# Performance work log

Hardware: AMD Instinct MI355X
Metric: run time of the kernel (lower is better)

## Reference

```python
import jax, jax.numpy as jnp
import numpy as np

B, T, C, H = 4, 2048, 1024, 16
HD = C // H
INIT_SCALE = 0.25

def setup_inputs() -> dict:
    key = jax.random.key(0)
    k1, k2, k3 = jax.random.split(key, 3)
    x = jax.random.normal(k1, (B, T, C), dtype=jnp.float32)
    W_attn = jax.random.normal(k2, (3 * C, C), dtype=jnp.float32) * INIT_SCALE  # torch Linear weight [out,in]
    b_attn = jnp.zeros((3 * C,), dtype=jnp.float32)
    W_proj = jax.random.normal(k3, (C, C), dtype=jnp.float32) * INIT_SCALE
    b_proj = jnp.zeros((C,), dtype=jnp.float32)
    return {"x": x, "W_attn": W_attn, "b_attn": b_attn, "W_proj": W_proj, "b_proj": b_proj}

def reference(x, W_attn, b_attn, W_proj, b_proj):
    # fused QKV projection: [B,T,3C]
    qkv = x @ W_attn.T + b_attn
    q, k, v = jnp.split(qkv, 3, axis=-1)  # each [B,T,C]
    # [B,H,T,HD]
    q = q.reshape(B, T, H, HD).transpose(0, 2, 1, 3)
    k = k.reshape(B, T, H, HD).transpose(0, 2, 1, 3)
    v = v.reshape(B, T, H, HD).transpose(0, 2, 1, 3)
    scale = 1.0 / jnp.sqrt(jnp.asarray(HD, dtype=q.dtype))
    attn = jnp.einsum('bhqd,bhkd->bhqk', q, k) * scale  # [B,H,T,T]
    attn = jax.nn.softmax(attn, axis=-1)
    out = jnp.einsum('bhqk,bhkd->bhqd', attn, v)  # [B,H,T,HD]
    out = out.transpose(0, 2, 1, 3).reshape(B, T, C)
    return out @ W_proj.T + b_proj
```

## Files before the change

### kernel.cpp

```cpp
#include <hip/hip_runtime.h>
#include <hip/hip_bf16.h>

#define BB 4
#define TT 2048
#define CC 1024
#define HH 16
#define HD 64

typedef _Float16 half8 __attribute__((ext_vector_type(8)));
typedef _Float16 half4 __attribute__((ext_vector_type(4)));
typedef _Float16 half2_t __attribute__((ext_vector_type(2)));
typedef __fp16 fp16x2 __attribute__((ext_vector_type(2)));
typedef float floatx4 __attribute__((ext_vector_type(4)));
typedef float floatx16 __attribute__((ext_vector_type(16)));
typedef int intx2 __attribute__((ext_vector_type(2)));
typedef int intx4 __attribute__((ext_vector_type(4)));

__device__ __forceinline__ void async_cp16(const void* g, void* l) {
    __builtin_amdgcn_global_load_lds(
        (const __attribute__((address_space(1))) unsigned int*)g,
        (__attribute__((address_space(3))) unsigned int*)l,
        16, 0, 0);
}

__device__ __forceinline__ float exp2_raw(float x) {
    return __builtin_amdgcn_exp2f(x);
}

__device__ __forceinline__ int pkh(float a, float b) {
    fp16x2 v = __builtin_amdgcn_cvt_pkrtz(a, b);
    return __builtin_bit_cast(int, v);
}

__device__ __forceinline__ float maxv16(floatx16 s) {
    float a0 = fmaxf(fmaxf(s[0], s[1]), s[2]);
    float a1 = fmaxf(fmaxf(s[3], s[4]), s[5]);
    float a2 = fmaxf(fmaxf(s[6], s[7]), s[8]);
    float a3 = fmaxf(fmaxf(s[9], s[10]), s[11]);
    float a4 = fmaxf(fmaxf(s[12], s[13]), s[14]);
    float b0 = fmaxf(fmaxf(a0, a1), a2);
    float b1 = fmaxf(fmaxf(a3, a4), s[15]);
    return fmaxf(b0, b1);
}

__device__ __forceinline__ half8 assembleF(int a, int b, int c, int d) {
    intx2 s1 = __builtin_amdgcn_permlane32_swap(a, c, false, false);
    intx2 s2 = __builtin_amdgcn_permlane32_swap(b, d, false, false);
    intx4 w = {s1[0], s2[0], s1[1], s2[1]};
    return __builtin_bit_cast(half8, w);
}

#define NX  (BB * TT * CC)
#define NWA (3 * CC * CC)
#define NWP (CC * CC)
__global__ void cvt_all(const float* __restrict__ x, const float* __restrict__ wa,
                        const float* __restrict__ wp,
                        _Float16* __restrict__ xh, _Float16* __restrict__ wah,
                        _Float16* __restrict__ wph) {
    int i = (blockIdx.x * blockDim.x + threadIdx.x) * 8;
    const float* src;
    _Float16* dst;
    int j;
    if (i < NX)            { src = x;  dst = xh;  j = i; }
    else if (i < NX + NWA) { src = wa; dst = wah; j = i - NX; }
    else                   { src = wp; dst = wph; j = i - NX - NWA; }
    float4 v0 = *(const float4*)(src + j);
    float4 v1 = *(const float4*)(src + j + 4);
    half8 h;
    h[0] = (_Float16)v0.x; h[1] = (_Float16)v0.y; h[2] = (_Float16)v0.z; h[3] = (_Float16)v0.w;
    h[4] = (_Float16)v1.x; h[5] = (_Float16)v1.y; h[6] = (_Float16)v1.z; h[7] = (_Float16)v1.w;
    *(half8*)(dst + j) = h;
}

template <int EPI>
__global__ __launch_bounds__(256) void hgemm_nt(
    const _Float16* __restrict__ A, const _Float16* __restrict__ Bw,
    const float* __restrict__ bias,
    _Float16* __restrict__ q_out, _Float16* __restrict__ k_out, _Float16* __restrict__ v_out,
    float* __restrict__ c_out,
    int M, int N, int K)
{
    __shared__ __attribute__((aligned(16))) _Float16 As[2 * 128 * 32];
    __shared__ __attribute__((aligned(16))) _Float16 Bs[2 * 128 * 32];

    const int tid  = threadIdx.x;
    const int lane = tid & 63;
    const int wave = tid >> 6;
    const int quad = lane >> 4;
    const int lc   = lane & 15;
    const int wr   = wave >> 1, wc = wave & 1;

    const int nwg = gridDim.x * gridDim.y;
    int flat = blockIdx.y * gridDim.x + blockIdx.x;
    flat = (flat & 7) * (nwg >> 3) + (flat >> 3);
    const size_t bm = (size_t)(flat / gridDim.x) * 128;
    const size_t bn = (size_t)(flat % gridDim.x) * 128;

    const int r0 = tid >> 2;
    const int ck = (tid & 3) * 8;

    const _Float16* Ap = A + (bm + r0) * (size_t)K + ck;
    const _Float16* Bp = Bw + (bn + r0) * (size_t)K + ck;
    _Float16* lA = As + tid * 8;
    _Float16* lB = Bs + tid * 8;
    const size_t rstep = (size_t)64 * K;

    floatx4 acc[4][4] = {};

    for (int kk = 0; kk < K; kk += 64) {
        __syncthreads();
        async_cp16(Ap + kk, lA);
        async_cp16(Ap + kk + rstep, lA + 2048);
        async_cp16(Ap + kk + 32, lA + 4096);
        async_cp16(Ap + kk + 32 + rstep, lA + 4096 + 2048);
        async_cp16(Bp + kk, lB);
        async_cp16(Bp + kk + rstep, lB + 2048);
        async_cp16(Bp + kk + 32, lB + 4096);
        async_cp16(Bp + kk + 32 + rstep, lB + 4096 + 2048);
        __syncthreads();

#pragma unroll
        for (int h = 0; h < 2; h++) {
            half8 af[4], bf[4];
#pragma unroll
            for (int mt = 0; mt < 4; mt++)
                af[mt] = *(const half8*)(As + h * 4096 + (wr * 64 + mt * 16 + lc) * 32 + quad * 8);
#pragma unroll
            for (int nt = 0; nt < 4; nt++)
                bf[nt] = *(const half8*)(Bs + h * 4096 + (wc * 64 + nt * 16 + lc) * 32 + quad * 8);
#pragma unroll
            for (int mt = 0; mt < 4; mt++)
#pragma unroll
                for (int nt = 0; nt < 4; nt++)
                    acc[mt][nt] = __builtin_amdgcn_mfma_f32_16x16x32_f16(af[mt], bf[nt], acc[mt][nt], 0, 0, 0);
        }
    }

#pragma unroll
    for (int mt = 0; mt < 4; mt++) {
        int mbase = (int)bm + wr * 64 + mt * 16 + quad * 4;
#pragma unroll
        for (int nt = 0; nt < 4; nt++) {
            int n = (int)bn + wc * 64 + nt * 16 + lc;
            float bv = bias[n];
#pragma unroll
            for (int r = 0; r < 4; r++) {
                float v = acc[mt][nt][r] + bv;
                int mm = mbase + r;
                if (EPI == 0) {
                    int seg = n >> 10;
                    int cm  = n & 1023;
                    int h = cm >> 6, d = cm & 63;
                    int bb = mm >> 11, t = mm & 2047;
                    size_t dst = (((size_t)(bb * HH + h)) * TT + t) * HD + d;
                    if (seg == 0)      q_out[dst] = (_Float16)(v * 0.18033688f);
                    else if (seg == 1) k_out[dst] = (_Float16)v;
                    else               v_out[dst] = (_Float16)v;
                } else {
                    c_out[(size_t)mm * N + n] = v;
                }
            }
        }
    }
}

__global__ __launch_bounds__(512) void attn_flash(
    const _Float16* __restrict__ Qp, const _Float16* __restrict__ Kp,
    const _Float16* __restrict__ Vp, _Float16* __restrict__ Op)
{
    __shared__ __attribute__((aligned(16))) _Float16 Ks[2][64 * 64];
    __shared__ __attribute__((aligned(16))) _Float16 Vt[2][64 * 64];

    const int bh   = blockIdx.x;
    const int qt   = blockIdx.y;
    const int tid  = threadIdx.x;
    const int lane = tid & 63;
    const int wave = tid >> 6;
    const int ql   = lane & 31;
    const int hi   = lane >> 5;

    const size_t hb = (size_t)bh * TT * HD;

    const int qrow = qt * 256 + wave * 32 + ql;
    half8 bq[4];
#pragma unroll
    for (int c = 0; c < 4; c++)
        bq[c] = *(const half8*)(Qp + hb + (size_t)qrow * HD + c * 16 + hi * 8);

    floatx16 o0 = (floatx16)0.0f, o1 = (floatx16)0.0f;
    float mrun = -1e30f, lrun = 0.f;

    const int sk = tid >> 3;
    const int sj = tid & 7;
    const int sg = sj ^ (sk & 7);
    const _Float16* Kg = Kp + hb + (size_t)sk * HD + sg * 8;

    const int vkp = tid >> 4;
    const int vd4 = (tid & 15) * 4;
    const _Float16* Vg0 = Vp + hb + (size_t)(2 * vkp) * HD + vd4;
    const _Float16* Vg1 = Vg0 + HD;

    half8 kv  = *(const half8*)Kg;
    half4 va0 = *(const half4*)Vg0;
    half4 vb0 = *(const half4*)Vg1;
    *(half8*)(Ks[0] + tid * 8) = kv;
#pragma unroll
    for (int j = 0; j < 4; j++) {
        int row = vd4 + j;
        int boff = (row * 128 + vkp * 4) ^ (((row >> 2) & 7) << 4);
        half2_t w; w[0] = va0[j]; w[1] = vb0[j];
        *(half2_t*)((char*)Vt[0] + boff) = w;
    }
    {
        const size_t koff = (size_t)64 * HD;
        kv  = *(const half8*)(Kg + koff);
        va0 = *(const half4*)(Vg0 + koff);
        vb0 = *(const half4*)(Vg1 + koff);
    }

    int cur = 0;
    for (int kt = 0; kt < TT; kt += 64) {
        __syncthreads();

        if (kt + 64 < TT) {
            *(half8*)(Ks[cur ^ 1] + tid * 8) = kv;
#pragma unroll
            for (int j = 0; j < 4; j++) {
                int row = vd4 + j;
                int boff = (row * 128 + vkp * 4) ^ (((row >> 2) & 7) << 4);
                half2_t w; w[0] = va0[j]; w[1] = vb0[j];
                *(half2_t*)((char*)Vt[cur ^ 1] + boff) = w;
            }
            if (kt + 128 < TT) {
                const size_t koff = (size_t)(kt + 128) * HD;
                kv  = *(const half8*)(Kg + koff);
                va0 = *(const half4*)(Vg0 + koff);
                vb0 = *(const half4*)(Vg1 + koff);
            }
        }

        const char* Kbuf = (const char*)Ks[cur];
        const char* Vbuf = (const char*)Vt[cur];

        floatx16 s0 = (floatx16)0.0f, s1 = (floatx16)0.0f;
        __builtin_amdgcn_s_setprio(1);
#pragma unroll
        for (int c = 0; c < 4; c++) {
            int offk = (ql * 128 + c * 32 + hi * 16) ^ ((ql & 7) << 4);
            half8 a0 = *(const half8*)(Kbuf + offk);
            half8 a1 = *(const half8*)(Kbuf + offk + 4096);
            s0 = __builtin_amdgcn_mfma_f32_32x32x16_f16(a0, bq[c], s0, 0, 0, 0);
            s1 = __builtin_amdgcn_mfma_f32_32x32x16_f16(a1, bq[c], s1, 0, 0, 0);
        }
        __builtin_amdgcn_s_setprio(0);

        float mx = fmaxf(maxv16(s0), maxv16(s1));
        mx = fmaxf(mx, __shfl_xor(mx, 32));
        const bool noresc = __all(mx <= mrun + 8.0f);
        const float mnew = noresc ? mrun : fmaxf(mrun, mx);
        float rs = 0.f;
        int d[16];
#pragma unroll
        for (int i = 0; i < 8; i++) {
            float e0 = exp2_raw(s0[2 * i] - mnew);
            float e1 = exp2_raw(s0[2 * i + 1] - mnew);
            rs += e0 + e1;
            d[i] = pkh(e0, e1);
        }
#pragma unroll
        for (int i = 0; i < 8; i++) {
            float e0 = exp2_raw(s1[2 * i] - mnew);
            float e1 = exp2_raw(s1[2 * i + 1] - mnew);
            rs += e0 + e1;
            d[8 + i] = pkh(e0, e1);
        }
        rs += __shfl_xor(rs, 32);
        if (!noresc) {
            float al = exp2_raw(mrun - mnew);
            mrun = mnew;
            lrun *= al;
            o0 *= al;
            o1 *= al;
        }
        lrun += rs;

        half8 F[4];
        F[0] = assembleF(d[0], d[1], d[2], d[3]);
        F[1] = assembleF(d[4], d[5], d[6], d[7]);
        F[2] = assembleF(d[8], d[9], d[10], d[11]);
        F[3] = assembleF(d[12], d[13], d[14], d[15]);

        __builtin_amdgcn_s_setprio(1);
#pragma unroll
        for (int kb = 0; kb < 4; kb++) {
            int offv = (ql * 128 + kb * 32 + hi * 16) ^ (((ql >> 2) & 7) << 4);
            half8 v0 = *(const half8*)(Vbuf + offv);
            half8 v1 = *(const half8*)(Vbuf + offv + 4096);
            o0 = __builtin_amdgcn_mfma_f32_32x32x16_f16(v0, F[kb], o0, 0, 0, 0);
            o1 = __builtin_amdgcn_mfma_f32_32x32x16_f16(v1, F[kb], o1, 0, 0, 0);
        }
        __builtin_amdgcn_s_setprio(0);

        cur ^= 1;
    }

    const float inv = __builtin_amdgcn_rcpf(lrun);
    const int b = bh >> 4, h = bh & 15;
    size_t base = ((size_t)(b * TT + qrow)) * CC + h * HD;
#pragma unroll
    for (int rr = 0; rr < 4; rr++) {
        half4 hv0, hv1;
#pragma unroll
        for (int t = 0; t < 4; t++) {
            hv0[t] = (_Float16)(o0[rr * 4 + t] * inv);
            hv1[t] = (_Float16)(o1[rr * 4 + t] * inv);
        }
        *(half4*)(Op + base + 8 * rr + 4 * hi) = hv0;
        *(half4*)(Op + base + 32 + 8 * rr + 4 * hi) = hv1;
    }
}

extern "C" void kernel_launch(void* const* d_in, const int* in_sizes, int n_in,
                              void* d_out, int out_size, void* d_ws, size_t ws_size,
                              hipStream_t stream) {
    const float* x      = (const float*)d_in[0];
    const float* W_attn = (const float*)d_in[1];
    const float* b_attn = (const float*)d_in[2];
    const float* W_proj = (const float*)d_in[3];
    const float* b_proj = (const float*)d_in[4];
    float* out = (float*)d_out;

    const size_t SZ_XH  = (size_t)BB * TT * CC * 2;
    const size_t SZ_WA  = (size_t)3 * CC * CC * 2;
    const size_t SZ_WP  = (size_t)CC * CC * 2;
    const size_t SZ_QKV = (size_t)BB * HH * TT * HD * 2;
    size_t off = 0;
    _Float16* xh  = (_Float16*)((char*)d_ws + off); off += SZ_XH;
    _Float16* wah = (_Float16*)((char*)d_ws + off); off += SZ_WA;
    _Float16* wph = (_Float16*)((char*)d_ws + off); off += SZ_WP;
    _Float16* Qh  = (_Float16*)((char*)d_ws + off); off += SZ_QKV;
    _Float16* Kh  = (_Float16*)((char*)d_ws + off); off += SZ_QKV;
    _Float16* Vh  = (_Float16*)((char*)d_ws + off); off += SZ_QKV;
    _Float16* Ah  = (_Float16*)((char*)d_ws + off); off += SZ_XH;
    if (ws_size < off) return;

    const int NTOT = NX + NWA + NWP;
    cvt_all<<<NTOT / 8 / 256, 256, 0, stream>>>(x, W_attn, W_proj, xh, wah, wph);

    hgemm_nt<0><<<dim3(3 * CC / 128, BB * TT / 128), 256, 0, stream>>>(
        xh, wah, b_attn, Qh, Kh, Vh, nullptr, BB * TT, 3 * CC, CC);

    attn_flash<<<dim3(BB * HH, TT / 256), 512, 0, stream>>>(Qh, Kh, Vh, Ah);

    hgemm_nt<1><<<dim3(CC / 128, BB * TT / 128), 256, 0, stream>>>(
        Ah, wph, b_proj, nullptr, nullptr, nullptr, out, BB * TT, CC, CC);
}
```

Measured before the change: 271.1 us.

## Store V transposed from QKV GEMM and triple-buffer K/V via async LDS loads

The QKV projection epilogue now writes V in [B,H,HD,T] layout, so the attention kernel no longer transposes V through registers. The attention kernel replaces its register-staged double buffer with a three-stage ring filled by global_load_lds async copies, waiting with vmcnt and a single barrier per tile. This targets VGPR staging and per-tile LDS write overhead and lets loads overlap compute two tiles ahead. The cost is more LDS (48KB), scattered strided V stores in the GEMM epilogue, and reliance on the ordering of the vmcnt counter.

```diff
diff --git a/kernel.cpp b/kernel.cpp
--- a/kernel.cpp
+++ b/kernel.cpp
@@ -152,10 +152,16 @@
                     int cm  = n & 1023;
                     int h = cm >> 6, d = cm & 63;
                     int bb = mm >> 11, t = mm & 2047;
-                    size_t dst = (((size_t)(bb * HH + h)) * TT + t) * HD + d;
-                    if (seg == 0)      q_out[dst] = (_Float16)(v * 0.18033688f);
-                    else if (seg == 1) k_out[dst] = (_Float16)v;
-                    else               v_out[dst] = (_Float16)v;
+                    if (seg == 0) {
+                        size_t dst = (((size_t)(bb * HH + h)) * TT + t) * HD + d;
+                        q_out[dst] = (_Float16)(v * 0.18033688f);
+                    } else if (seg == 1) {
+                        size_t dst = (((size_t)(bb * HH + h)) * TT + t) * HD + d;
+                        k_out[dst] = (_Float16)v;
+                    } else {
+                        size_t dst = (((size_t)(bb * HH + h)) * HD + d) * TT + t;
+                        v_out[dst] = (_Float16)v;
+                    }
                 } else {
                     c_out[(size_t)mm * N + n] = v;
                 }
@@ -166,10 +172,10 @@
 
 __global__ __launch_bounds__(512) void attn_flash(
     const _Float16* __restrict__ Qp, const _Float16* __restrict__ Kp,
-    const _Float16* __restrict__ Vp, _Float16* __restrict__ Op)
+    const _Float16* __restrict__ Vtp, _Float16* __restrict__ Op)
 {
-    __shared__ __attribute__((aligned(16))) _Float16 Ks[2][64 * 64];
-    __shared__ __attribute__((aligned(16))) _Float16 Vt[2][64 * 64];
+    __shared__ __attribute__((aligned(16))) _Float16 Ks[3][64 * 64];
+    __shared__ __attribute__((aligned(16))) _Float16 Vs[3][64 * 64];
 
     const int bh   = blockIdx.x;
     const int qt   = blockIdx.y;
@@ -190,57 +196,37 @@
     floatx16 o0 = (floatx16)0.0f, o1 = (floatx16)0.0f;
     float mrun = -1e30f, lrun = 0.f;
 
-    const int sk = tid >> 3;
-    const int sj = tid & 7;
-    const int sg = sj ^ (sk & 7);
-    const _Float16* Kg = Kp + hb + (size_t)sk * HD + sg * 8;
-
-    const int vkp = tid >> 4;
-    const int vd4 = (tid & 15) * 4;
-    const _Float16* Vg0 = Vp + hb + (size_t)(2 * vkp) * HD + vd4;
-    const _Float16* Vg1 = Vg0 + HD;
-
-    half8 kv  = *(const half8*)Kg;
-    half4 va0 = *(const half4*)Vg0;
-    half4 vb0 = *(const half4*)Vg1;
-    *(half8*)(Ks[0] + tid * 8) = kv;
-#pragma unroll
-    for (int j = 0; j < 4; j++) {
-        int row = vd4 + j;
-        int boff = (row * 128 + vkp * 4) ^ (((row >> 2) & 7) << 4);
-        half2_t w; w[0] = va0[j]; w[1] = vb0[j];
-        *(half2_t*)((char*)Vt[0] + boff) = w;
-    }
-    {
-        const size_t koff = (size_t)64 * HD;
-        kv  = *(const half8*)(Kg + koff);
-        va0 = *(const half4*)(Vg0 + koff);
-        vb0 = *(const half4*)(Vg1 + koff);
-    }
-
-    int cur = 0;
-    for (int kt = 0; kt < TT; kt += 64) {
-        __syncthreads();
-
-        if (kt + 64 < TT) {
-            *(half8*)(Ks[cur ^ 1] + tid * 8) = kv;
-#pragma unroll
-            for (int j = 0; j < 4; j++) {
-                int row = vd4 + j;
-                int boff = (row * 128 + vkp * 4) ^ (((row >> 2) & 7) << 4);
-                half2_t w; w[0] = va0[j]; w[1] = vb0[j];
-                *(half2_t*)((char*)Vt[cur ^ 1] + boff) = w;
-            }
-            if (kt + 128 < TT) {
-                const size_t koff = (size_t)(kt + 128) * HD;
-                kv  = *(const half8*)(Kg + koff);
-                va0 = *(const half4*)(Vg0 + koff);
-                vb0 = *(const half4*)(Vg1 + koff);
-            }
-        }
-
-        const char* Kbuf = (const char*)Ks[cur];
-        const char* Vbuf = (const char*)Vt[cur];
+    const int srow = tid >> 3;
+    const int sgk  = (tid & 7) ^ (srow & 7);
+    const int sgv  = (tid & 7) ^ ((srow >> 2) & 7);
+    const _Float16* Kg = Kp  + hb + (size_t)srow * HD + sgk * 8;
+    const _Float16* Vg = Vtp + hb + (size_t)srow * TT + sgv * 8;
+
+    asm volatile("s_waitcnt vmcnt(0)" ::: "memory");
+    __builtin_amdgcn_sched_barrier(0);
+
+    async_cp16(Kg,           Ks[0] + tid * 8);
+    async_cp16(Vg,           Vs[0] + tid * 8);
+    async_cp16(Kg + 64 * HD, Ks[1] + tid * 8);
+    async_cp16(Vg + 64,      Vs[1] + tid * 8);
+
+    const int NT = TT / 64;
+    for (int t = 0; t < NT; ++t) {
+        if (t < NT - 1) asm volatile("s_waitcnt vmcnt(2)" ::: "memory");
+        else            asm volatile("s_waitcnt vmcnt(0)" ::: "memory");
+        __builtin_amdgcn_s_barrier();
+        __builtin_amdgcn_sched_barrier(0);
+
+        if (t + 2 < NT) {
+            const int q = (t + 2) - ((t + 2) / 3) * 3;
+            async_cp16(Kg + (size_t)(t + 2) * 64 * HD, Ks[q] + tid * 8);
+            async_cp16(Vg + (t + 2) * 64,              Vs[q] + tid * 8);
+        }
+        __builtin_amdgcn_sched_barrier(0);
+
+        const int cb = t - (t / 3) * 3;
+        const char* Kbuf = (const char*)Ks[cb];
+        const char* Vbuf = (const char*)Vs[cb];
 
         floatx16 s0 = (floatx16)0.0f, s1 = (floatx16)0.0f;
         __builtin_amdgcn_s_setprio(1);
@@ -300,8 +286,6 @@
             o1 = __builtin_amdgcn_mfma_f32_32x32x16_f16(v1, F[kb], o1, 0, 0, 0);
         }
         __builtin_amdgcn_s_setprio(0);
-
-        cur ^= 1;
     }
 
     const float inv = __builtin_amdgcn_rcpf(lrun);
```

Result: slower. 298.7 us (+10.2%).

## Replace QKV GEMM with 256x256-tile eight-phase pipelined kernel

Applied to the files above, without the earlier changes.

The QKV projection moves from the generic 128x128 hgemm to a dedicated 512-thread kernel with 256x256 tiles and a K-step of 64. Each tile is split into four 128x128 quadrants processed in eight phases, with async global-to-LDS copies interleaved between them, XOR-swizzled LDS reads, and raised wave priority around the MFMA blocks. The goal is more data reuse per LDS load and better overlap of memory traffic with MFMA work. In exchange the kernel uses much more LDS and registers (one block per CU) and launches only 384 blocks, which may hurt load balance. The projection GEMM becomes a non-templated copy of the old kernel.

```diff
diff --git a/kernel.cpp b/kernel.cpp
--- a/kernel.cpp
+++ b/kernel.cpp
@@ -72,12 +72,147 @@
     *(half8*)(dst + j) = h;
 }
 
-template <int EPI>
-__global__ __launch_bounds__(256) void hgemm_nt(
+__global__ __launch_bounds__(512, 1) void qkv8ph(
     const _Float16* __restrict__ A, const _Float16* __restrict__ Bw,
     const float* __restrict__ bias,
-    _Float16* __restrict__ q_out, _Float16* __restrict__ k_out, _Float16* __restrict__ v_out,
-    float* __restrict__ c_out,
+    _Float16* __restrict__ q_out, _Float16* __restrict__ k_out, _Float16* __restrict__ v_out)
+{
+    __shared__ __attribute__((aligned(16))) _Float16 LA[2 * 256 * 64];
+    __shared__ __attribute__((aligned(16))) _Float16 LB[2 * 256 * 64];
+
+    const int tid  = threadIdx.x;
+    const int lane = tid & 63;
+    const int wave = tid >> 6;
+    const int quad = lane >> 4;
+    const int lc   = lane & 15;
+    const int wr   = wave >> 2;
+    const int wn   = wave & 3;
+
+    int flat = blockIdx.y * gridDim.x + blockIdx.x;
+    flat = (flat & 7) * 48 + (flat >> 3);
+    const size_t bm = (size_t)(flat / 12) * 256;
+    const size_t bn = (size_t)(flat % 12) * 256;
+
+    const int srow = tid >> 3;
+    const int sch  = (tid & 7) ^ (srow & 7);
+    const _Float16* Asrc = A  + (bm + srow) * (size_t)CC + sch * 8;
+    const _Float16* Bsrc = Bw + (bn + srow) * (size_t)CC + sch * 8;
+    const int xr = lc & 7;
+
+    floatx4 acc[2][4][2][2] = {};
+    half8 af[4][2], bf[2][2];
+
+#define STG_A(BOFF, H, T) do { if ((T) < 16) {                                        \
+        async_cp16(Asrc + (size_t)((H) * 128) * CC + (T) * 64,                        \
+                   LA + (BOFF) + (H) * 8192 + tid * 8);                               \
+        async_cp16(Asrc + (size_t)((H) * 128 + 64) * CC + (T) * 64,                   \
+                   LA + (BOFF) + (H) * 8192 + 4096 + tid * 8); } } while (0)
+#define STG_B(BOFF, H, T) do { if ((T) < 16) {                                        \
+        async_cp16(Bsrc + (size_t)((H) * 128) * CC + (T) * 64,                        \
+                   LB + (BOFF) + (H) * 8192 + tid * 8);                               \
+        async_cp16(Bsrc + (size_t)((H) * 128 + 64) * CC + (T) * 64,                   \
+                   LB + (BOFF) + (H) * 8192 + 4096 + tid * 8); } } while (0)
+#define RD_A(BOFF, MQ) do {                                                           \
+        _Pragma("unroll") for (int mt = 0; mt < 4; mt++) {                            \
+            int row = (MQ) * 128 + wr * 64 + mt * 16 + lc;                            \
+            _Pragma("unroll") for (int kh = 0; kh < 2; kh++)                          \
+                af[mt][kh] = *(const half8*)(LA + (BOFF) + row * 64 +                 \
+                                             ((kh * 4 + quad) ^ xr) * 8);             \
+        } } while (0)
+#define RD_B(BOFF, NQ) do {                                                           \
+        _Pragma("unroll") for (int nt = 0; nt < 2; nt++) {                            \
+            int row = (NQ) * 128 + wn * 32 + nt * 16 + lc;                            \
+            _Pragma("unroll") for (int kh = 0; kh < 2; kh++)                          \
+                bf[nt][kh] = *(const half8*)(LB + (BOFF) + row * 64 +                 \
+                                             ((kh * 4 + quad) ^ xr) * 8);             \
+        } } while (0)
+#define DO_MFMA(MQ, NQ) do {                                                          \
+        __builtin_amdgcn_s_setprio(1);                                                \
+        _Pragma("unroll") for (int mt = 0; mt < 4; mt++)                              \
+        _Pragma("unroll") for (int nt = 0; nt < 2; nt++) {                            \
+            acc[MQ][mt][NQ][nt] = __builtin_amdgcn_mfma_f32_16x16x32_f16(             \
+                af[mt][0], bf[nt][0], acc[MQ][mt][NQ][nt], 0, 0, 0);                  \
+            acc[MQ][mt][NQ][nt] = __builtin_amdgcn_mfma_f32_16x16x32_f16(             \
+                af[mt][1], bf[nt][1], acc[MQ][mt][NQ][nt], 0, 0, 0);                  \
+        }                                                                             \
+        __builtin_amdgcn_s_setprio(0);                                                \
+    } while (0)
+#define MIDBAR() do { __builtin_amdgcn_s_barrier();                                   \
+        asm volatile("s_waitcnt lgkmcnt(0)" ::: "memory");                            \
+        __builtin_amdgcn_sched_barrier(0); } while (0)
+#define ENDBAR() __builtin_amdgcn_s_barrier()
+#define VMW(N) do { asm volatile("s_waitcnt vmcnt(" #N ")" ::: "memory");             \
+        __builtin_amdgcn_sched_barrier(0); } while (0)
+
+    STG_A(0, 0, 0); STG_A(0, 1, 0); STG_B(0, 0, 0); STG_B(0, 1, 0);
+    STG_A(16384, 0, 1); STG_B(16384, 1, 1);
+    VMW(4);
+    __builtin_amdgcn_s_barrier();
+
+#pragma unroll 1
+    for (int i = 0; i < 8; ++i) {
+        const int tb = 2 * i + 1, ta2 = 2 * i + 2, tb2 = 2 * i + 3;
+        RD_A(0, 0); RD_B(0, 0); STG_A(16384, 1, tb);
+        MIDBAR(); DO_MFMA(0, 0); ENDBAR();
+        RD_B(0, 1); STG_B(16384, 0, tb);
+        MIDBAR(); DO_MFMA(0, 1); ENDBAR();
+        RD_A(0, 1); STG_A(0, 0, ta2);
+        MIDBAR(); DO_MFMA(1, 1); ENDBAR();
+        RD_B(0, 0); STG_B(0, 1, ta2);
+        MIDBAR(); DO_MFMA(1, 0);
+        if (i < 7) { VMW(4); } else { VMW(0); }
+        ENDBAR();
+        RD_A(16384, 0); RD_B(16384, 0); STG_A(0, 1, ta2);
+        MIDBAR(); DO_MFMA(0, 0); ENDBAR();
+        RD_B(16384, 1); STG_B(0, 0, ta2);
+        MIDBAR(); DO_MFMA(0, 1); ENDBAR();
+        RD_A(16384, 1); STG_A(16384, 0, tb2);
+        MIDBAR(); DO_MFMA(1, 1); ENDBAR();
+        RD_B(16384, 0); STG_B(16384, 1, tb2);
+        MIDBAR(); DO_MFMA(1, 0);
+        if (i < 7) { VMW(4); }
+        ENDBAR();
+    }
+#undef STG_A
+#undef STG_B
+#undef RD_A
+#undef RD_B
+#undef DO_MFMA
+#undef MIDBAR
+#undef ENDBAR
+#undef VMW
+
+#pragma unroll
+    for (int mq = 0; mq < 2; mq++)
+#pragma unroll
+    for (int mt = 0; mt < 4; mt++) {
+        int mbase = (int)bm + mq * 128 + wr * 64 + mt * 16 + quad * 4;
+#pragma unroll
+        for (int nq = 0; nq < 2; nq++)
+#pragma unroll
+        for (int nt = 0; nt < 2; nt++) {
+            int n = (int)bn + nq * 128 + wn * 32 + nt * 16 + lc;
+            float bv = bias[n];
+#pragma unroll
+            for (int r = 0; r < 4; r++) {
+                float v = acc[mq][mt][nq][nt][r] + bv;
+                int mm = mbase + r;
+                int seg = n >> 10;
+                int cm  = n & 1023;
+                int hh = cm >> 6, d = cm & 63;
+                int b2 = mm >> 11, t = mm & 2047;
+                size_t dst = (((size_t)(b2 * HH + hh)) * TT + t) * HD + d;
+                if (seg == 0)      q_out[dst] = (_Float16)(v * 0.18033688f);
+                else if (seg == 1) k_out[dst] = (_Float16)v;
+                else               v_out[dst] = (_Float16)v;
+            }
+        }
+    }
+}
+
+__global__ __launch_bounds__(256) void hgemm_proj(
+    const _Float16* __restrict__ A, const _Float16* __restrict__ Bw,
+    const float* __restrict__ bias, float* __restrict__ c_out,
     int M, int N, int K)
 {
     __shared__ __attribute__((aligned(16))) _Float16 As[2 * 128 * 32];
@@ -144,22 +279,8 @@
             int n = (int)bn + wc * 64 + nt * 16 + lc;
             float bv = bias[n];
 #pragma unroll
-            for (int r = 0; r < 4; r++) {
-                float v = acc[mt][nt][r] + bv;
-                int mm = mbase + r;
-                if (EPI == 0) {
-                    int seg = n >> 10;
-                    int cm  = n & 1023;
-                    int h = cm >> 6, d = cm & 63;
-                    int bb = mm >> 11, t = mm & 2047;
-                    size_t dst = (((size_t)(bb * HH + h)) * TT + t) * HD + d;
-                    if (seg == 0)      q_out[dst] = (_Float16)(v * 0.18033688f);
-                    else if (seg == 1) k_out[dst] = (_Float16)v;
-                    else               v_out[dst] = (_Float16)v;
-                } else {
-                    c_out[(size_t)mm * N + n] = v;
-                }
-            }
+            for (int r = 0; r < 4; r++)
+                c_out[(size_t)(mbase + r) * N + n] = acc[mt][nt][r] + bv;
         }
     }
 }
@@ -347,11 +468,10 @@
     const int NTOT = NX + NWA + NWP;
     cvt_all<<<NTOT / 8 / 256, 256, 0, stream>>>(x, W_attn, W_proj, xh, wah, wph);
 
-    hgemm_nt<0><<<dim3(3 * CC / 128, BB * TT / 128), 256, 0, stream>>>(
-        xh, wah, b_attn, Qh, Kh, Vh, nullptr, BB * TT, 3 * CC, CC);
+    qkv8ph<<<dim3(12, 32), 512, 0, stream>>>(xh, wah, b_attn, Qh, Kh, Vh);
 
     attn_flash<<<dim3(BB * HH, TT / 256), 512, 0, stream>>>(Qh, Kh, Vh, Ah);
 
-    hgemm_nt<1><<<dim3(CC / 128, BB * TT / 128), 256, 0, stream>>>(
-        Ah, wph, b_proj, nullptr, nullptr, nullptr, out, BB * TT, CC, CC);
-}
+    hgemm_proj<<<dim3(CC / 128, BB * TT / 128), 256, 0, stream>>>(
+        Ah, wph, b_proj, out, BB * TT, CC, CC);
+}
```

After: 270.5 us. About the same (-0.2%).
